# Optimization experiments

Measured on AMD Instinct MI355X. Metric: run time of the kernel, lower is better.

Reference implementation:

```python
import jax, jax.numpy as jnp
import numpy as np

B, NP, FIN = 128, 64, 2048   # graphs, nodes per graph, input feat
H, D = 8, 64                 # GAT heads, per-head dim
HD = H * D                   # 512
HID = 1024                   # Set2Set channels (concat of two 512 convs)
R2 = 16.0                    # radius^2 (r=4)
SLOPE = 0.2                  # GATConv leaky_relu slope
EPS = 0.1                    # BatchNorm eps


def setup_inputs() -> dict:
    key = jax.random.key(0)
    ks = jax.random.split(key, 20)
    s = 0.02
    inp = {}
    inp['x'] = jax.random.normal(ks[0], (B * NP, FIN), jnp.float32)
    inp['pos'] = jax.random.uniform(ks[1], (B * NP, 2), jnp.float32) * 20.0
    inp['batch'] = jnp.repeat(jnp.arange(B, dtype=jnp.int32), NP)
    # lin01: Linear(2048,2048,bias=False) + BN(2048, eps=0.1) (eval mode)
    inp['W0'] = jax.random.normal(ks[2], (FIN, 2048), jnp.float32) * s
    inp['bn0_g'] = jnp.ones((2048,), jnp.float32)
    inp['bn0_b'] = jnp.zeros((2048,), jnp.float32)
    inp['bn0_m'] = jnp.zeros((2048,), jnp.float32)
    inp['bn0_v'] = jnp.ones((2048,), jnp.float32)
    # two GATConv(2048, 64, heads=8)
    inp['Wg1'] = jax.random.normal(ks[3], (2048, HD), jnp.float32) * s
    inp['as1'] = jax.random.normal(ks[4], (H, D), jnp.float32) * s
    inp['ad1'] = jax.random.normal(ks[5], (H, D), jnp.float32) * s
    inp['b1'] = jnp.zeros((HD,), jnp.float32)
    inp['Wg2'] = jax.random.normal(ks[6], (2048, HD), jnp.float32) * s
    inp['as2'] = jax.random.normal(ks[7], (H, D), jnp.float32) * s
    inp['ad2'] = jax.random.normal(ks[8], (H, D), jnp.float32) * s
    inp['b2'] = jnp.zeros((HD,), jnp.float32)
    # Set2Set LSTM: 2 layers, input 2*HID, hidden HID
    inp['Wih0'] = jax.random.normal(ks[9], (4 * HID, 2 * HID), jnp.float32) * s
    inp['Whh0'] = jax.random.normal(ks[10], (4 * HID, HID), jnp.float32) * s
    inp['bih0'] = jnp.zeros((4 * HID,), jnp.float32)
    inp['bhh0'] = jnp.zeros((4 * HID,), jnp.float32)
    inp['Wih1'] = jax.random.normal(ks[11], (4 * HID, HID), jnp.float32) * s
    inp['Whh1'] = jax.random.normal(ks[12], (4 * HID, HID), jnp.float32) * s
    inp['bih1'] = jnp.zeros((4 * HID,), jnp.float32)
    inp['bhh1'] = jnp.zeros((4 * HID,), jnp.float32)
    # lin2: Linear(2048,1024,bias=False) + BN(1024, eps=0.1)
    inp['W2'] = jax.random.normal(ks[13], (2 * HID, HID), jnp.float32) * s
    inp['bn2_g'] = jnp.ones((HID,), jnp.float32)
    inp['bn2_b'] = jnp.zeros((HID,), jnp.float32)
    inp['bn2_m'] = jnp.zeros((HID,), jnp.float32)
    inp['bn2_v'] = jnp.ones((HID,), jnp.float32)
    # lin3: Linear(1024, 10)
    inp['W3'] = jax.random.normal(ks[14], (HID, 10), jnp.float32) * s
    inp['b3'] = jnp.zeros((10,), jnp.float32)
    return inp


def _bn(x, g, b, m, v):
    return (x - m) * jax.lax.rsqrt(v + EPS) * g + b


def _gat(xb, adj, Wg, a_src, a_dst, bias):
    # xb: [B, NP, 2048], adj: [B, NP, NP] bool (diag True = self-loops)
    h = (xb @ Wg).reshape(B, NP, H, D)
    es = jnp.einsum('bnhd,hd->bnh', h, a_src)   # source-node score
    ed = jnp.einsum('bnhd,hd->bnh', h, a_dst)   # target-node score
    # e[b, i, j, h]: edge j -> i
    e = jax.nn.leaky_relu(ed[:, :, None, :] + es[:, None, :, :], SLOPE)
    e = jnp.where(adj[..., None], e, -jnp.inf)
    alpha = jax.nn.softmax(e, axis=2)           # softmax over neighbors j
    out = jnp.einsum('bijh,bjhd->bihd', alpha, h).reshape(B, NP, HD)
    return out + bias


def _cell(inp, h, c, Wih, Whh, bih, bhh):
    z = inp @ Wih.T + h @ Whh.T + bih + bhh
    i, f, g, o = jnp.split(z, 4, axis=-1)
    c = jax.nn.sigmoid(f) * c + jax.nn.sigmoid(i) * jnp.tanh(g)
    return jax.nn.sigmoid(o) * jnp.tanh(c), c


def _forward(x, pos, W0, bn0_g, bn0_b, bn0_m, bn0_v,
             Wg1, as1, ad1, b1, Wg2, as2, ad2, b2,
             Wih0, Whh0, bih0, bhh0, Wih1, Whh1, bih1, bhh1,
             W2, bn2_g, bn2_b, bn2_m, bn2_v, W3, b3):
    # radius_graph(r=4) per graph; GATConv re-adds self-loops -> diag True
    p = pos.reshape(B, NP, 2)
    d2 = jnp.sum((p[:, :, None, :] - p[:, None, :, :]) ** 2, axis=-1)
    adj = d2 <= R2
    x = _bn(jax.nn.relu(x @ W0), bn0_g, bn0_b, bn0_m, bn0_v)  # dropout: eval
    xb = x.reshape(B, NP, 2048)
    g1 = jax.nn.relu(_gat(xb, adj, Wg1, as1, ad1, b1))
    g2 = jax.nn.relu(_gat(xb, adj, Wg2, as2, ad2, b2))
    x2 = jnp.concatenate([g1, g2], axis=-1)                   # [B, NP, 1024]
    # Set2Set: processing_steps=2, 2-layer LSTM
    q_star = jnp.zeros((B, 2 * HID), x2.dtype)
    h0 = c0 = h1 = c1 = jnp.zeros((B, HID), x2.dtype)
    for _ in range(2):
        h0, c0 = _cell(q_star, h0, c0, Wih0, Whh0, bih0, bhh0)
        h1, c1 = _cell(h0, h1, c1, Wih1, Whh1, bih1, bhh1)
        e = jnp.einsum('bnd,bd->bn', x2, h1)
        a = jax.nn.softmax(e, axis=1)                         # per-graph softmax
        r = jnp.einsum('bn,bnd->bd', a, x2)
        q_star = jnp.concatenate([h1, r], axis=-1)            # [B, 2048]
    y = _bn(jax.nn.relu(q_star @ W2), bn2_g, bn2_b, bn2_m, bn2_v)
    return y @ W3 + b3                                        # [B, 10] ('A2')


def reference(x, pos, batch, W0, bn0_g, bn0_b, bn0_m, bn0_v,
              Wg1, as1, ad1, b1, Wg2, as2, ad2, b2,
              Wih0, Whh0, bih0, bhh0, Wih1, Whh1, bih1, bhh1,
              W2, bn2_g, bn2_b, bn2_m, bn2_v, W3, b3):
    # batch ids are implicit in the fixed [B, NP] layout
    return _forward(x, pos, W0, bn0_g, bn0_b, bn0_m, bn0_v,
                    Wg1, as1, ad1, b1, Wg2, as2, ad2, b2,
                    Wih0, Whh0, bih0, bhh0, Wih1, Whh1, bih1, bhh1,
                    W2, bn2_g, bn2_b, bn2_m, bn2_v, W3, b3)
```

## Files before the change

kernel.cpp:

```cpp
#include <hip/hip_runtime.h>
#include <hip/hip_bf16.h>

typedef unsigned short u16;
typedef __attribute__((ext_vector_type(8))) short short8;
typedef __attribute__((ext_vector_type(4))) float f32x4;
typedef unsigned long long u64;

#define DI __device__ __forceinline__

DI u16 f2b(float f){
  unsigned u = __float_as_uint(f);
  unsigned r = 0x7fffu + ((u >> 16) & 1u);
  return (u16)((u + r) >> 16);
}
DI float b2f(u16 u){ return __uint_as_float((unsigned)u << 16); }

DI void gl_lds16(const void* g, void* l){
  __builtin_amdgcn_global_load_lds((const __attribute__((address_space(1))) void*)g,
                                   (__attribute__((address_space(3))) void*)l, 16, 0, 0);
}

constexpr size_t O_XBF = 0;
constexpr size_t O_W0T = O_XBF + 33554432;
constexpr size_t O_WGT = O_W0T + 8388608;
constexpr size_t O_W2T = O_WGT + 4194304;
constexpr size_t O_LW0 = O_W2T + 4194304;
constexpr size_t O_LW1 = O_LW0 + 25165824;
constexpr size_t O_XB  = O_LW1 + 16777216;
constexpr size_t O_H   = O_XB  + 33554432;
constexpr size_t O_ES  = O_H   + 33554432;
constexpr size_t O_ED  = O_ES  + 524288;
constexpr size_t O_ADJ = O_ED  + 524288;
constexpr size_t O_SC0 = O_ADJ + 65536;
constexpr size_t O_SH0 = O_SC0 + 8192;
constexpr size_t O_SC2 = O_SH0 + 8192;
constexpr size_t O_SH2 = O_SC2 + 4096;
constexpr size_t O_LB0 = O_SH2 + 4096;
constexpr size_t O_LB1 = O_LB0 + 16384;
constexpr size_t S_AC0 = 0;
constexpr size_t S_AC1 = S_AC0 + 786432;
constexpr size_t S_C0  = S_AC1 + 524288;
constexpr size_t S_C1  = S_C0  + 524288;
constexpr size_t S_H1F = S_C1  + 524288;
constexpr size_t S_ZP  = S_H1F + 524288;
constexpr size_t S_E   = S_ZP  + 16777216;
constexpr size_t S_H0U = S_E   + 32768;
constexpr size_t S_Z1U = S_H0U + 4096;

__global__ __launch_bounds__(256) void cvt_big(
    const float* __restrict__ x, const float* __restrict__ Wih0, const float* __restrict__ Whh0,
    const float* __restrict__ Wih1, const float* __restrict__ Whh1,
    u16* __restrict__ xbf, u16* __restrict__ lw0, u16* __restrict__ lw1){
  int bx = blockIdx.x;
  int idx, cq, dld, doff;
  const float* src; u16* dst;
  if(bx < 16384){      src = x;    dst = xbf; idx = bx * 256 + threadIdx.x;            cq = 512; dld = 2048; doff = 0; }
  else if(bx < 24576){ src = Wih0; dst = lw0; idx = (bx - 16384) * 256 + threadIdx.x;  cq = 512; dld = 3072; doff = 0; }
  else if(bx < 28672){ src = Whh0; dst = lw0; idx = (bx - 24576) * 256 + threadIdx.x;  cq = 256; dld = 3072; doff = 2048; }
  else if(bx < 32768){ src = Wih1; dst = lw1; idx = (bx - 28672) * 256 + threadIdx.x;  cq = 256; dld = 2048; doff = 0; }
  else {               src = Whh1; dst = lw1; idx = (bx - 32768) * 256 + threadIdx.x;  cq = 256; dld = 2048; doff = 1024; }
  int r = idx / cq, c4 = (idx - r * cq) << 2;
  float4 v = *(const float4*)(src + (size_t)r * (cq << 2) + c4);
  u16 o[4] = { f2b(v.x), f2b(v.y), f2b(v.z), f2b(v.w) };
  *(ushort4*)(dst + (size_t)r * dld + doff + c4) = *(ushort4*)o;
}

__global__ void cvt_tr(const float* __restrict__ W0, const float* __restrict__ Wg1,
                       const float* __restrict__ Wg2, const float* __restrict__ W2,
                       u16* __restrict__ w0t, u16* __restrict__ wgt, u16* __restrict__ w2t){
  __shared__ float tile[32][33];
  int bx = blockIdx.x;
  const float* src; u16* dst; int C, droff;
  if(bx < 64){      src = W0;  dst = w0t; C = 2048; droff = 0; }
  else if(bx < 80){ src = Wg1; dst = wgt; C = 512;  droff = 0;   bx -= 64; }
  else if(bx < 96){ src = Wg2; dst = wgt; C = 512;  droff = 512; bx -= 80; }
  else {            src = W2;  dst = w2t; C = 1024; droff = 0;   bx -= 96; }
  int c0 = bx * 32, r0 = blockIdx.y * 32;
  int tx = threadIdx.x, ty = threadIdx.y;
  for(int i = 0; i < 4; i++)
    tile[ty + 8*i][tx] = src[(size_t)(r0 + ty + 8*i) * C + c0 + tx];
  __syncthreads();
  for(int i = 0; i < 4; i++)
    dst[(size_t)(droff + c0 + ty + 8*i) * 2048 + r0 + tx] = f2b(tile[tx][ty + 8*i]);
}

__global__ void prep(const float* g0, const float* b0, const float* m0, const float* v0,
                     const float* g2, const float* b2, const float* m2, const float* v2,
                     const float* bih0, const float* bhh0, const float* bih1, const float* bhh1,
                     float* sc0, float* sh0, float* sc2, float* sh2, float* lb0, float* lb1){
  int t = blockIdx.x * 256 + threadIdx.x;
  if(t < 2048){ float s = g0[t] * rsqrtf(v0[t] + 0.1f); sc0[t] = s; sh0[t] = b0[t] - m0[t] * s; }
  if(t < 1024){ float s = g2[t] * rsqrtf(v2[t] + 0.1f); sc2[t] = s; sh2[t] = b2[t] - m2[t] * s; }
  if(t < 4096){ lb0[t] = bih0[t] + bhh0[t]; lb1[t] = bih1[t] + bhh1[t]; }
}

__global__ void adj_kernel(const float* __restrict__ pos, u64* __restrict__ adjm){
  int b = blockIdx.x, l = threadIdx.x;
  __shared__ float px[64], py[64];
  float2 p = ((const float2*)pos)[b * 64 + l];
  px[l] = p.x; py[l] = p.y;
  __syncthreads();
  float xi = px[l], yi = py[l];
  u64 m = 0;
  for(int j = 0; j < 64; j++){
    float dx = xi - px[j], dy = yi - py[j];
    if(dx * dx + dy * dy <= 16.0f) m |= (1ull << j);
  }
  adjm[b * 64 + l] = m;
}

template<int MODE>
__global__ __launch_bounds__(256) void gemm_bf16(
    const u16* __restrict__ A, const u16* __restrict__ Bt,
    float* __restrict__ Cf, u16* __restrict__ Cb,
    const float* __restrict__ p1, const float* __restrict__ p2,
    int M, int N, int K)
{
  constexpr int BM = 128, BN = 128, BK = 64;
  __shared__ alignas(16) u16 Al[BM * BK];
  __shared__ alignas(16) u16 Bl[BN * BK];
  int m0 = blockIdx.x * BM, n0 = blockIdx.y * BN;
  int t = threadIdx.x, w = t >> 6, l = t & 63;
  int wm = (w >> 1) * 64, wn = (w & 1) * 64;
  f32x4 acc[4][4];
  for(int a = 0; a < 4; a++) for(int b = 0; b < 4; b++) acc[a][b] = {0.f, 0.f, 0.f, 0.f};

  const short8* Ap = (const short8*)Al;
  const short8* Bp = (const short8*)Bl;

  for(int k0 = 0; k0 < K; k0 += BK){
    #pragma unroll
    for(int u = t; u < BM * 8; u += 256){
      int r = u >> 3, c = u & 7;
      gl_lds16(A + (size_t)(m0 + r) * K + k0 + ((c ^ (r & 7)) << 3), Al + u * 8);
    }
    #pragma unroll
    for(int u = t; u < BN * 8; u += 256){
      int r = u >> 3, c = u & 7;
      gl_lds16(Bt + (size_t)(n0 + r) * K + k0 + ((c ^ (r & 7)) << 3), Bl + u * 8);
    }
    __syncthreads();
    #pragma unroll
    for(int ks = 0; ks < 2; ks++){
      int kc = ks * 4 + (l >> 4);
      short8 av[4], bv[4];
      #pragma unroll
      for(int mi = 0; mi < 4; mi++){ int r = wm + mi * 16 + (l & 15); av[mi] = Ap[r * 8 + (kc ^ (r & 7))]; }
      #pragma unroll
      for(int ni = 0; ni < 4; ni++){ int r = wn + ni * 16 + (l & 15); bv[ni] = Bp[r * 8 + (kc ^ (r & 7))]; }
      #pragma unroll
      for(int mi = 0; mi < 4; mi++)
        #pragma unroll
        for(int ni = 0; ni < 4; ni++)
          acc[mi][ni] = __builtin_amdgcn_mfma_f32_16x16x32_bf16(av[mi], bv[ni], acc[mi][ni], 0, 0, 0);
    }
    __syncthreads();
  }

  int cr = m0 + wm + ((l >> 4) << 2);
  int cc = n0 + wn + (l & 15);
  for(int mi = 0; mi < 4; mi++)
    for(int ni = 0; ni < 4; ni++)
      for(int r = 0; r < 4; r++){
        int row = cr + mi * 16 + r, col = cc + ni * 16;
        float v = acc[mi][ni][r];
        if(MODE == 1){ v = fmaxf(v, 0.f) * p1[col] + p2[col]; Cb[(size_t)row * N + col] = f2b(v); }
        else if(MODE == 3){ Cb[(size_t)row * N + col] = f2b(v); }
        else { Cf[(size_t)row * N + col] = v; }
      }
}

__global__ __launch_bounds__(256) void gemm_sk(
    const u16* __restrict__ A, const u16* __restrict__ Bt, float* __restrict__ Cf,
    int N, int lda, int ldb, int kPer)
{
  constexpr int BM = 128, BN = 64, BK = 64;
  __shared__ alignas(16) u16 Al[BM * BK];
  __shared__ alignas(16) u16 Bl[BN * BK];
  int n0 = blockIdx.x * BN;
  int kb = blockIdx.y * kPer;
  float* C = Cf + (size_t)blockIdx.y * 128 * N;
  int t = threadIdx.x, w = t >> 6, l = t & 63;
  int wm = (w >> 1) * 64, wn = (w & 1) * 32;
  f32x4 acc[4][2];
  for(int a = 0; a < 4; a++) for(int b = 0; b < 2; b++) acc[a][b] = {0.f, 0.f, 0.f, 0.f};

  const short8* Ap = (const short8*)Al;
  const short8* Bp = (const short8*)Bl;

  for(int k0 = kb; k0 < kb + kPer; k0 += BK){
    #pragma unroll
    for(int u = t; u < BM * 8; u += 256){
      int r = u >> 3, c = u & 7;
      gl_lds16(A + (size_t)r * lda + k0 + ((c ^ (r & 7)) << 3), Al + u * 8);
    }
    #pragma unroll
    for(int u = t; u < BN * 8; u += 256){
      int r = u >> 3, c = u & 7;
      gl_lds16(Bt + (size_t)(n0 + r) * ldb + k0 + ((c ^ (r & 7)) << 3), Bl + u * 8);
    }
    __syncthreads();
    #pragma unroll
    for(int ks = 0; ks < 2; ks++){
      int kc = ks * 4 + (l >> 4);
      short8 av[4], bv[2];
      #pragma unroll
      for(int mi = 0; mi < 4; mi++){ int r = wm + mi * 16 + (l & 15); av[mi] = Ap[r * 8 + (kc ^ (r & 7))]; }
      #pragma unroll
      for(int ni = 0; ni < 2; ni++){ int r = wn + ni * 16 + (l & 15); bv[ni] = Bp[r * 8 + (kc ^ (r & 7))]; }
      #pragma unroll
      for(int mi = 0; mi < 4; mi++)
        #pragma unroll
        for(int ni = 0; ni < 2; ni++)
          acc[mi][ni] = __builtin_amdgcn_mfma_f32_16x16x32_bf16(av[mi], bv[ni], acc[mi][ni], 0, 0, 0);
    }
    __syncthreads();
  }

  int cr = wm + ((l >> 4) << 2);
  int cc = n0 + wn + (l & 15);
  for(int mi = 0; mi < 4; mi++)
    for(int ni = 0; ni < 2; ni++)
      for(int r = 0; r < 4; r++)
        C[(size_t)(cr + mi * 16 + r) * N + cc + ni * 16] = acc[mi][ni][r];
}

__global__ __launch_bounds__(256) void gat_scores(const u16* __restrict__ h,
    const float* __restrict__ as1, const float* __restrict__ ad1,
    const float* __restrict__ as2, const float* __restrict__ ad2,
    float* __restrict__ es, float* __restrict__ ed){
  __shared__ float aS[16][64], aD[16][64];
  int t = threadIdx.x;
  for(int i = t; i < 1024; i += 256){
    int cc = i >> 6, d = i & 63;
    aS[cc][d] = (cc < 8) ? as1[i] : as2[i - 512];
    aD[cc][d] = (cc < 8) ? ad1[i] : ad2[i - 512];
  }
  __syncthreads();
  int w = t >> 6, l = t & 63;
  int node = blockIdx.x * 4 + w;
  const u16* hr = h + (size_t)node * 1024;
  for(int cc = 0; cc < 16; cc++){
    float v = b2f(hr[cc * 64 + l]);
    float ps = v * aS[cc][l], pd = v * aD[cc][l];
    for(int o = 32; o; o >>= 1){ ps += __shfl_down(ps, o); pd += __shfl_down(pd, o); }
    if(l == 0){ es[node * 16 + cc] = ps; ed[node * 16 + cc] = pd; }
  }
}

__global__ __launch_bounds__(256) void gat_attn2(const u64* __restrict__ adjm,
    const float* __restrict__ es, const float* __restrict__ ed,
    const u16* __restrict__ h, const float* __restrict__ b1, const float* __restrict__ b2,
    float* __restrict__ x2){
  int b = blockIdx.x;
  int cv = blockIdx.y >> 3, hh = blockIdx.y & 7;
  __shared__ float hst[64][64];
  __shared__ float alphaL[64][65];
  __shared__ float esl[64], edl[64];
  __shared__ u64 adjs[64];
  int t = threadIdx.x, w = t >> 6, l = t & 63;
  {
    int j = t >> 2, d0 = (t & 3) * 16;
    const u16* hr = h + (size_t)(b * 64 + j) * 1024 + cv * 512 + hh * 64 + d0;
    #pragma unroll
    for(int k = 0; k < 16; k++) hst[j][d0 + k] = b2f(hr[k]);
  }
  if(t < 64){
    esl[t] = es[(b * 64 + t) * 16 + cv * 8 + hh];
    edl[t] = ed[(b * 64 + t) * 16 + cv * 8 + hh];
    adjs[t] = adjm[b * 64 + t];
  }
  __syncthreads();
  for(int it = 0; it < 16; it++){
    int i = it * 4 + w;
    bool on = (adjs[i] >> l) & 1;
    float e = edl[i] + esl[l];
    e = e > 0.f ? e : 0.2f * e;
    float mx = on ? e : -1e30f;
    for(int o = 32; o; o >>= 1) mx = fmaxf(mx, __shfl_xor(mx, o));
    float p = on ? __expf(e - mx) : 0.f;
    float s = p;
    for(int o = 32; o; o >>= 1) s += __shfl_xor(s, o);
    alphaL[i][l] = p / s;
  }
  __syncthreads();
  int i = t >> 2, q = t & 3;
  float acc[16];
  #pragma unroll
  for(int k = 0; k < 16; k++) acc[k] = 0.f;
  for(int j = 0; j < 64; j++){
    float al = alphaL[i][j];
    const float* hr = &hst[j][q * 16];
    #pragma unroll
    for(int k = 0; k < 16; k++) acc[k] += al * hr[k];
  }
  const float* bias = (cv ? b2 : b1) + hh * 64 + q * 16;
  float* op = x2 + (size_t)(b * 64 + i) * 1024 + cv * 512 + hh * 64 + q * 16;
  #pragma unroll
  for(int k = 0; k < 16; k += 4){
    float4 o;
    o.x = fmaxf(acc[k] + bias[k], 0.f);
    o.y = fmaxf(acc[k+1] + bias[k+1], 0.f);
    o.z = fmaxf(acc[k+2] + bias[k+2], 0.f);
    o.w = fmaxf(acc[k+3] + bias[k+3], 0.f);
    *(float4*)(op + k) = o;
  }
}

__global__ void s2s0_h0(const float* __restrict__ lb0, float* __restrict__ h0u){
  int j = blockIdx.x * 256 + threadIdx.x;
  if(j >= 1024) return;
  float zi = lb0[j], zg = lb0[2048 + j], zo = lb0[3072 + j];
  float si = 1.f / (1.f + __expf(-zi));
  float so = 1.f / (1.f + __expf(-zo));
  float cn = si * tanhf(zg);
  h0u[j] = so * tanhf(cn);
}

__global__ __launch_bounds__(256) void s2s0_gemv(const float* __restrict__ Wih1,
    const float* __restrict__ lb1, const float* __restrict__ h0u, float* __restrict__ z1u){
  __shared__ float hs[1024];
  int t = threadIdx.x;
  for(int i = t; i < 1024; i += 256) hs[i] = h0u[i];
  __syncthreads();
  int w = t >> 6, l = t & 63;
  int r = blockIdx.x * 4 + w;
  const float* wr = Wih1 + (size_t)r * 1024;
  float s = 0.f;
  #pragma unroll
  for(int k = 0; k < 16; k++) s += wr[l + 64 * k] * hs[l + 64 * k];
  for(int o = 32; o; o >>= 1) s += __shfl_xor(s, o);
  if(l == 0) z1u[r] = s + lb1[r];
}

__global__ void s2s0_bcast(const float* __restrict__ lb0, const float* __restrict__ z1u,
    float* __restrict__ c0b, float* __restrict__ c1b, float* __restrict__ h1f,
    u16* __restrict__ ac0, u16* __restrict__ ac1){
  int t = blockIdx.x * 256 + threadIdx.x;
  int b = t >> 10, j = t & 1023;
  float zi0 = lb0[j], zg0 = lb0[2048 + j], zo0 = lb0[3072 + j];
  float c0 = (1.f / (1.f + __expf(-zi0))) * tanhf(zg0);
  float h0 = (1.f / (1.f + __expf(-zo0))) * tanhf(c0);
  float zi1 = z1u[j], zg1 = z1u[2048 + j], zo1 = z1u[3072 + j];
  float c1 = (1.f / (1.f + __expf(-zi1))) * tanhf(zg1);
  float h1 = (1.f / (1.f + __expf(-zo1))) * tanhf(c1);
  c0b[t] = c0;
  c1b[t] = c1;
  h1f[t] = h1;
  u16 h0b = f2b(h0), h1b = f2b(h1);
  ac0[(size_t)b * 3072 + j] = h1b;
  ac0[(size_t)b * 3072 + 2048 + j] = h0b;
  ac1[(size_t)b * 2048 + j] = h0b;
  ac1[(size_t)b * 2048 + 1024 + j] = h1b;
}

__global__ void lstm_gate0(const float* __restrict__ zp, const float* __restrict__ lb,
                           float* __restrict__ c, u16* __restrict__ ac0, u16* __restrict__ ac1,
                           int ns){
  int t = blockIdx.x * 256 + threadIdx.x;
  int b = t >> 10, j = t & 1023;
  size_t base = (size_t)b * 4096;
  float zi = 0, zf = 0, zg = 0, zo = 0;
  for(int s = 0; s < ns; s++){
    const float* zr = zp + (size_t)s * 524288 + base;
    zi += zr[j]; zf += zr[1024 + j]; zg += zr[2048 + j]; zo += zr[3072 + j];
  }
  zi += lb[j]; zf += lb[1024 + j]; zg += lb[2048 + j]; zo += lb[3072 + j];
  float ci = c[t];
  float si = 1.f / (1.f + __expf(-zi)), sf = 1.f / (1.f + __expf(-zf)), so = 1.f / (1.f + __expf(-zo));
  float cn = sf * ci + si * tanhf(zg);
  c[t] = cn;
  u16 hb = f2b(so * tanhf(cn));
  ac0[(size_t)b * 3072 + 2048 + j] = hb;
  ac1[(size_t)b * 2048 + j] = hb;
}

__global__ void lstm_gate1(const float* __restrict__ zp, const float* __restrict__ lb,
                           float* __restrict__ c, float* __restrict__ h1f,
                           u16* __restrict__ ac1, u16* __restrict__ ac0, int ns){
  int t = blockIdx.x * 256 + threadIdx.x;
  int b = t >> 10, j = t & 1023;
  size_t base = (size_t)b * 4096;
  float zi = 0, zf = 0, zg = 0, zo = 0;
  for(int s = 0; s < ns; s++){
    const float* zr = zp + (size_t)s * 524288 + base;
    zi += zr[j]; zf += zr[1024 + j]; zg += zr[2048 + j]; zo += zr[3072 + j];
  }
  zi += lb[j]; zf += lb[1024 + j]; zg += lb[2048 + j]; zo += lb[3072 + j];
  float ci = c[t];
  float si = 1.f / (1.f + __expf(-zi)), sf = 1.f / (1.f + __expf(-zf)), so = 1.f / (1.f + __expf(-zo));
  float cn = sf * ci + si * tanhf(zg);
  c[t] = cn;
  float hn = so * tanhf(cn);
  h1f[t] = hn;
  u16 hb = f2b(hn);
  ac1[(size_t)b * 2048 + 1024 + j] = hb;
  ac0[(size_t)b * 3072 + j] = hb;
}

__global__ __launch_bounds__(256) void s2s_e(const float* __restrict__ x2,
    const float* __restrict__ h1, float* __restrict__ e){
  int t = threadIdx.x, w = t >> 6, l = t & 63;
  int node = blockIdx.x * 4 + w;
  int b = node >> 6;
  const float4* xr = (const float4*)(x2 + (size_t)node * 1024);
  const float4* hr = (const float4*)(h1 + (size_t)b * 1024);
  float s = 0.f;
  #pragma unroll
  for(int k = 0; k < 4; k++){
    float4 a = xr[l + 64 * k], c = hr[l + 64 * k];
    s += a.x * c.x + a.y * c.y + a.z * c.z + a.w * c.w;
  }
  for(int o = 32; o; o >>= 1) s += __shfl_xor(s, o);
  if(l == 0) e[node] = s;
}

__global__ __launch_bounds__(256) void s2s_r(const float* __restrict__ x2,
    const float* __restrict__ e, u16* __restrict__ ac0){
  int b = blockIdx.x, sl = blockIdx.y;
  __shared__ float al[64];
  int t = threadIdx.x;
  if(t < 64){
    float v = e[b * 64 + t];
    float mx = v;
    for(int o = 32; o; o >>= 1) mx = fmaxf(mx, __shfl_xor(mx, o));
    float p = __expf(v - mx);
    float ss = p;
    for(int o = 32; o; o >>= 1) ss += __shfl_xor(ss, o);
    al[t] = p / ss;
  }
  __syncthreads();
  int d = sl * 256 + t;
  const float* xp = x2 + (size_t)b * 64 * 1024 + d;
  float r = 0.f;
  #pragma unroll 8
  for(int j = 0; j < 64; j++) r += al[j] * xp[j * 1024];
  ac0[(size_t)b * 3072 + 1024 + d] = f2b(r);
}

__global__ __launch_bounds__(256) void lin3(const float* __restrict__ zp2,
    const float* __restrict__ sc2, const float* __restrict__ sh2,
    const float* __restrict__ W3, const float* __restrict__ b3, float* __restrict__ out){
  int b = blockIdx.x;
  __shared__ float yl[1024];
  int t = threadIdx.x, w = t >> 6, l = t & 63;
  for(int d = t; d < 1024; d += 256){
    float v = 0.f;
    for(int s = 0; s < 8; s++) v += zp2[(size_t)s * 131072 + b * 1024 + d];
    yl[d] = fmaxf(v, 0.f) * sc2[d] + sh2[d];
  }
  __syncthreads();
  for(int n = w; n < 10; n += 4){
    float s = 0.f;
    for(int d = l; d < 1024; d += 64) s += yl[d] * W3[d * 10 + n];
    for(int o = 32; o; o >>= 1) s += __shfl_xor(s, o);
    if(l == 0) out[b * 10 + n] = s + b3[n];
  }
}

extern "C" void kernel_launch(void* const* d_in, const int* in_sizes, int n_in,
                              void* d_out, int out_size, void* d_ws, size_t ws_size,
                              hipStream_t stream){
  const float* x    = (const float*)d_in[0];
  const float* pos  = (const float*)d_in[1];
  const float* W0   = (const float*)d_in[3];
  const float* bn0g = (const float*)d_in[4];
  const float* bn0b = (const float*)d_in[5];
  const float* bn0m = (const float*)d_in[6];
  const float* bn0v = (const float*)d_in[7];
  const float* Wg1  = (const float*)d_in[8];
  const float* as1  = (const float*)d_in[9];
  const float* ad1  = (const float*)d_in[10];
  const float* b1   = (const float*)d_in[11];
  const float* Wg2  = (const float*)d_in[12];
  const float* as2  = (const float*)d_in[13];
  const float* ad2  = (const float*)d_in[14];
  const float* b2   = (const float*)d_in[15];
  const float* Wih0 = (const float*)d_in[16];
  const float* Whh0 = (const float*)d_in[17];
  const float* bih0 = (const float*)d_in[18];
  const float* bhh0 = (const float*)d_in[19];
  const float* Wih1 = (const float*)d_in[20];
  const float* Whh1 = (const float*)d_in[21];
  const float* bih1 = (const float*)d_in[22];
  const float* bhh1 = (const float*)d_in[23];
  const float* W2   = (const float*)d_in[24];
  const float* bn2g = (const float*)d_in[25];
  const float* bn2b = (const float*)d_in[26];
  const float* bn2m = (const float*)d_in[27];
  const float* bn2v = (const float*)d_in[28];
  const float* W3   = (const float*)d_in[29];
  const float* b3   = (const float*)d_in[30];

  char* ws = (char*)d_ws;
  u16*   xbf  = (u16*)(ws + O_XBF);
  float* x2   = (float*)(ws + O_XBF);
  u16*   w0t  = (u16*)(ws + O_W0T);
  u16*   wgt  = (u16*)(ws + O_WGT);
  u16*   w2t  = (u16*)(ws + O_W2T);
  u16*   lw0  = (u16*)(ws + O_LW0);
  u16*   lw1  = (u16*)(ws + O_LW1);
  u16*   xb   = (u16*)(ws + O_XB);
  u16*   hb   = (u16*)(ws + O_H);
  float* es   = (float*)(ws + O_ES);
  float* ed   = (float*)(ws + O_ED);
  u64*   adjm = (u64*)(ws + O_ADJ);
  float* sc0  = (float*)(ws + O_SC0);
  float* sh0  = (float*)(ws + O_SH0);
  float* sc2  = (float*)(ws + O_SC2);
  float* sh2  = (float*)(ws + O_SH2);
  float* lb0  = (float*)(ws + O_LB0);
  float* lb1  = (float*)(ws + O_LB1);
  char*  s2sb = ws + O_H;
  u16*   ac0  = (u16*)(s2sb + S_AC0);
  u16*   ac1  = (u16*)(s2sb + S_AC1);
  float* c0b  = (float*)(s2sb + S_C0);
  float* c1b  = (float*)(s2sb + S_C1);
  float* h1f  = (float*)(s2sb + S_H1F);
  float* zp   = (float*)(s2sb + S_ZP);
  float* ebuf = (float*)(s2sb + S_E);
  float* h0u  = (float*)(s2sb + S_H0U);
  float* z1u  = (float*)(s2sb + S_Z1U);

  prep<<<16, 256, 0, stream>>>(bn0g, bn0b, bn0m, bn0v, bn2g, bn2b, bn2m, bn2v,
                               bih0, bhh0, bih1, bhh1, sc0, sh0, sc2, sh2, lb0, lb1);
  adj_kernel<<<128, 64, 0, stream>>>(pos, adjm);
  cvt_big<<<36864, 256, 0, stream>>>(x, Wih0, Whh0, Wih1, Whh1, xbf, lw0, lw1);
  cvt_tr<<<dim3(128, 64), dim3(32, 8), 0, stream>>>(W0, Wg1, Wg2, W2, w0t, wgt, w2t);

  gemm_bf16<1><<<dim3(64, 16), 256, 0, stream>>>(xbf, w0t, nullptr, xb, sc0, sh0, 8192, 2048, 2048);
  gemm_bf16<3><<<dim3(64, 8), 256, 0, stream>>>(xb, wgt, nullptr, hb, nullptr, nullptr, 8192, 1024, 2048);
  gat_scores<<<2048, 256, 0, stream>>>(hb, as1, ad1, as2, ad2, es, ed);
  gat_attn2<<<dim3(128, 16), 256, 0, stream>>>(adjm, es, ed, hb, b1, b2, x2);

  s2s0_h0<<<4, 256, 0, stream>>>(lb0, h0u);
  s2s0_gemv<<<1024, 256, 0, stream>>>(Wih1, lb1, h0u, z1u);
  s2s0_bcast<<<512, 256, 0, stream>>>(lb0, z1u, c0b, c1b, h1f, ac0, ac1);
  s2s_e<<<2048, 256, 0, stream>>>(x2, h1f, ebuf);
  s2s_r<<<dim3(128, 4), 256, 0, stream>>>(x2, ebuf, ac0);

  gemm_sk<<<dim3(64, 8), 256, 0, stream>>>(ac0, lw0, zp, 4096, 3072, 3072, 384);
  lstm_gate0<<<512, 256, 0, stream>>>(zp, lb0, c0b, ac0, ac1, 8);
  gemm_sk<<<dim3(64, 8), 256, 0, stream>>>(ac1, lw1, zp, 4096, 2048, 2048, 256);
  lstm_gate1<<<512, 256, 0, stream>>>(zp, lb1, c1b, h1f, ac1, ac0, 8);
  s2s_e<<<2048, 256, 0, stream>>>(x2, h1f, ebuf);
  s2s_r<<<dim3(128, 4), 256, 0, stream>>>(x2, ebuf, ac0);

  gemm_sk<<<dim3(16, 8), 256, 0, stream>>>(ac0, w2t, zp, 1024, 3072, 2048, 256);
  lin3<<<128, 256, 0, stream>>>(zp, sc2, sh2, W3, b3, (float*)d_out);
}
```

Baseline: 340.4 us.

## Fuse LSTM weight bf16 conversion into split-K GEMM and store GAT output as bf16

Drops the separate pass that converted the LSTM weight matrices to bf16. A new split-K GEMM loads the fp32 Wih/Whh weights directly, converts them in registers and writes them into LDS. This removes a large convert-and-write step and the re-read of its output. The GAT attention output x2 is now stored as bf16, which halves the traffic for the Set2Set e/r kernels but adds rounding error. The new B load is synchronous and uses two float4 loads per 16 bytes of bf16, which may slow the GEMM's inner loop.

```diff
diff --git a/kernel.cpp b/kernel.cpp
--- a/kernel.cpp
+++ b/kernel.cpp
@@ -24,9 +24,7 @@
 constexpr size_t O_W0T = O_XBF + 33554432;
 constexpr size_t O_WGT = O_W0T + 8388608;
 constexpr size_t O_W2T = O_WGT + 4194304;
-constexpr size_t O_LW0 = O_W2T + 4194304;
-constexpr size_t O_LW1 = O_LW0 + 25165824;
-constexpr size_t O_XB  = O_LW1 + 16777216;
+constexpr size_t O_XB  = O_W2T + 4194304;
 constexpr size_t O_H   = O_XB  + 33554432;
 constexpr size_t O_ES  = O_H   + 33554432;
 constexpr size_t O_ED  = O_ES  + 524288;
@@ -47,22 +45,12 @@
 constexpr size_t S_H0U = S_E   + 32768;
 constexpr size_t S_Z1U = S_H0U + 4096;
 
-__global__ __launch_bounds__(256) void cvt_big(
-    const float* __restrict__ x, const float* __restrict__ Wih0, const float* __restrict__ Whh0,
-    const float* __restrict__ Wih1, const float* __restrict__ Whh1,
-    u16* __restrict__ xbf, u16* __restrict__ lw0, u16* __restrict__ lw1){
-  int bx = blockIdx.x;
-  int idx, cq, dld, doff;
-  const float* src; u16* dst;
-  if(bx < 16384){      src = x;    dst = xbf; idx = bx * 256 + threadIdx.x;            cq = 512; dld = 2048; doff = 0; }
-  else if(bx < 24576){ src = Wih0; dst = lw0; idx = (bx - 16384) * 256 + threadIdx.x;  cq = 512; dld = 3072; doff = 0; }
-  else if(bx < 28672){ src = Whh0; dst = lw0; idx = (bx - 24576) * 256 + threadIdx.x;  cq = 256; dld = 3072; doff = 2048; }
-  else if(bx < 32768){ src = Wih1; dst = lw1; idx = (bx - 28672) * 256 + threadIdx.x;  cq = 256; dld = 2048; doff = 0; }
-  else {               src = Whh1; dst = lw1; idx = (bx - 32768) * 256 + threadIdx.x;  cq = 256; dld = 2048; doff = 1024; }
-  int r = idx / cq, c4 = (idx - r * cq) << 2;
-  float4 v = *(const float4*)(src + (size_t)r * (cq << 2) + c4);
+__global__ __launch_bounds__(256) void cvt_x(const float* __restrict__ x, u16* __restrict__ xbf){
+  int idx = blockIdx.x * 256 + threadIdx.x;
+  int r = idx >> 9, c4 = (idx & 511) << 2;
+  float4 v = *(const float4*)(x + (size_t)r * 2048 + c4);
   u16 o[4] = { f2b(v.x), f2b(v.y), f2b(v.z), f2b(v.w) };
-  *(ushort4*)(dst + (size_t)r * dld + doff + c4) = *(ushort4*)o;
+  *(ushort4*)(xbf + (size_t)r * 2048 + c4) = *(ushort4*)o;
 }
 
 __global__ void cvt_tr(const float* __restrict__ W0, const float* __restrict__ Wg1,
@@ -225,6 +213,69 @@
         C[(size_t)(cr + mi * 16 + r) * N + cc + ni * 16] = acc[mi][ni][r];
 }
 
+__global__ __launch_bounds__(256) void gemm_skf(
+    const u16* __restrict__ A, const float* __restrict__ Wih, const float* __restrict__ Whh,
+    float* __restrict__ Cf, int N, int lda, int Kih, int Khh, int kPer)
+{
+  constexpr int BM = 128, BN = 64, BK = 64;
+  __shared__ alignas(16) u16 Al[BM * BK];
+  __shared__ alignas(16) u16 Bl[BN * BK];
+  int n0 = blockIdx.x * BN;
+  int kb = blockIdx.y * kPer;
+  float* C = Cf + (size_t)blockIdx.y * 128 * N;
+  int t = threadIdx.x, w = t >> 6, l = t & 63;
+  int wm = (w >> 1) * 64, wn = (w & 1) * 32;
+  f32x4 acc[4][2];
+  for(int a = 0; a < 4; a++) for(int b = 0; b < 2; b++) acc[a][b] = {0.f, 0.f, 0.f, 0.f};
+
+  const short8* Ap = (const short8*)Al;
+  const short8* Bp = (const short8*)Bl;
+
+  for(int k0 = kb; k0 < kb + kPer; k0 += BK){
+    #pragma unroll
+    for(int u = t; u < BM * 8; u += 256){
+      int r = u >> 3, c = u & 7;
+      gl_lds16(A + (size_t)r * lda + k0 + ((c ^ (r & 7)) << 3), Al + u * 8);
+    }
+    #pragma unroll
+    for(int u = t; u < BN * 8; u += 256){
+      int r = u >> 3, c = u & 7;
+      int gk = k0 + c * 8;
+      const float* src = (gk < Kih) ? (Wih + (size_t)(n0 + r) * Kih + gk)
+                                    : (Whh + (size_t)(n0 + r) * Khh + (gk - Kih));
+      float4 v0 = *(const float4*)src;
+      float4 v1 = *(const float4*)(src + 4);
+      short8 ov;
+      ov[0] = (short)f2b(v0.x); ov[1] = (short)f2b(v0.y); ov[2] = (short)f2b(v0.z); ov[3] = (short)f2b(v0.w);
+      ov[4] = (short)f2b(v1.x); ov[5] = (short)f2b(v1.y); ov[6] = (short)f2b(v1.z); ov[7] = (short)f2b(v1.w);
+      ((short8*)Bl)[r * 8 + (c ^ (r & 7))] = ov;
+    }
+    __syncthreads();
+    #pragma unroll
+    for(int ks = 0; ks < 2; ks++){
+      int kc = ks * 4 + (l >> 4);
+      short8 av[4], bv[2];
+      #pragma unroll
+      for(int mi = 0; mi < 4; mi++){ int r = wm + mi * 16 + (l & 15); av[mi] = Ap[r * 8 + (kc ^ (r & 7))]; }
+      #pragma unroll
+      for(int ni = 0; ni < 2; ni++){ int r = wn + ni * 16 + (l & 15); bv[ni] = Bp[r * 8 + (kc ^ (r & 7))]; }
+      #pragma unroll
+      for(int mi = 0; mi < 4; mi++)
+        #pragma unroll
+        for(int ni = 0; ni < 2; ni++)
+          acc[mi][ni] = __builtin_amdgcn_mfma_f32_16x16x32_bf16(av[mi], bv[ni], acc[mi][ni], 0, 0, 0);
+    }
+    __syncthreads();
+  }
+
+  int cr = wm + ((l >> 4) << 2);
+  int cc = n0 + wn + (l & 15);
+  for(int mi = 0; mi < 4; mi++)
+    for(int ni = 0; ni < 2; ni++)
+      for(int r = 0; r < 4; r++)
+        C[(size_t)(cr + mi * 16 + r) * N + cc + ni * 16] = acc[mi][ni][r];
+}
+
 __global__ __launch_bounds__(256) void gat_scores(const u16* __restrict__ h,
     const float* __restrict__ as1, const float* __restrict__ ad1,
     const float* __restrict__ as2, const float* __restrict__ ad2,
@@ -251,7 +302,7 @@
 __global__ __launch_bounds__(256) void gat_attn2(const u64* __restrict__ adjm,
     const float* __restrict__ es, const float* __restrict__ ed,
     const u16* __restrict__ h, const float* __restrict__ b1, const float* __restrict__ b2,
-    float* __restrict__ x2){
+    u16* __restrict__ x2b){
   int b = blockIdx.x;
   int cv = blockIdx.y >> 3, hh = blockIdx.y & 7;
   __shared__ float hst[64][64];
@@ -295,16 +346,9 @@
     for(int k = 0; k < 16; k++) acc[k] += al * hr[k];
   }
   const float* bias = (cv ? b2 : b1) + hh * 64 + q * 16;
-  float* op = x2 + (size_t)(b * 64 + i) * 1024 + cv * 512 + hh * 64 + q * 16;
+  u16* op = x2b + (size_t)(b * 64 + i) * 1024 + cv * 512 + hh * 64 + q * 16;
   #pragma unroll
-  for(int k = 0; k < 16; k += 4){
-    float4 o;
-    o.x = fmaxf(acc[k] + bias[k], 0.f);
-    o.y = fmaxf(acc[k+1] + bias[k+1], 0.f);
-    o.z = fmaxf(acc[k+2] + bias[k+2], 0.f);
-    o.w = fmaxf(acc[k+3] + bias[k+3], 0.f);
-    *(float4*)(op + k) = o;
-  }
+  for(int k = 0; k < 16; k++) op[k] = f2b(fmaxf(acc[k] + bias[k], 0.f));
 }
 
 __global__ void s2s0_h0(const float* __restrict__ lb0, float* __restrict__ h0u){
@@ -398,24 +442,24 @@
   ac0[(size_t)b * 3072 + j] = hb;
 }
 
-__global__ __launch_bounds__(256) void s2s_e(const float* __restrict__ x2,
+__global__ __launch_bounds__(256) void s2s_e(const u16* __restrict__ x2b,
     const float* __restrict__ h1, float* __restrict__ e){
   int t = threadIdx.x, w = t >> 6, l = t & 63;
   int node = blockIdx.x * 4 + w;
   int b = node >> 6;
-  const float4* xr = (const float4*)(x2 + (size_t)node * 1024);
-  const float4* hr = (const float4*)(h1 + (size_t)b * 1024);
+  const u16* xr = x2b + (size_t)node * 1024;
+  const float* hr = h1 + (size_t)b * 1024;
   float s = 0.f;
   #pragma unroll
-  for(int k = 0; k < 4; k++){
-    float4 a = xr[l + 64 * k], c = hr[l + 64 * k];
-    s += a.x * c.x + a.y * c.y + a.z * c.z + a.w * c.w;
+  for(int k = 0; k < 16; k++){
+    int d = k * 64 + l;
+    s += b2f(xr[d]) * hr[d];
   }
   for(int o = 32; o; o >>= 1) s += __shfl_xor(s, o);
   if(l == 0) e[node] = s;
 }
 
-__global__ __launch_bounds__(256) void s2s_r(const float* __restrict__ x2,
+__global__ __launch_bounds__(256) void s2s_r(const u16* __restrict__ x2b,
     const float* __restrict__ e, u16* __restrict__ ac0){
   int b = blockIdx.x, sl = blockIdx.y;
   __shared__ float al[64];
@@ -431,10 +475,10 @@
   }
   __syncthreads();
   int d = sl * 256 + t;
-  const float* xp = x2 + (size_t)b * 64 * 1024 + d;
+  const u16* xp = x2b + (size_t)b * 65536 + d;
   float r = 0.f;
   #pragma unroll 8
-  for(int j = 0; j < 64; j++) r += al[j] * xp[j * 1024];
+  for(int j = 0; j < 64; j++) r += al[j] * b2f(xp[j * 1024]);
   ac0[(size_t)b * 3072 + 1024 + d] = f2b(r);
 }
 
@@ -494,12 +538,10 @@
 
   char* ws = (char*)d_ws;
   u16*   xbf  = (u16*)(ws + O_XBF);
-  float* x2   = (float*)(ws + O_XBF);
+  u16*   x2b  = (u16*)(ws + O_XBF);
   u16*   w0t  = (u16*)(ws + O_W0T);
   u16*   wgt  = (u16*)(ws + O_WGT);
   u16*   w2t  = (u16*)(ws + O_W2T);
-  u16*   lw0  = (u16*)(ws + O_LW0);
-  u16*   lw1  = (u16*)(ws + O_LW1);
   u16*   xb   = (u16*)(ws + O_XB);
   u16*   hb   = (u16*)(ws + O_H);
   float* es   = (float*)(ws + O_ES);
@@ -525,26 +567,26 @@
   prep<<<16, 256, 0, stream>>>(bn0g, bn0b, bn0m, bn0v, bn2g, bn2b, bn2m, bn2v,
                                bih0, bhh0, bih1, bhh1, sc0, sh0, sc2, sh2, lb0, lb1);
   adj_kernel<<<128, 64, 0, stream>>>(pos, adjm);
-  cvt_big<<<36864, 256, 0, stream>>>(x, Wih0, Whh0, Wih1, Whh1, xbf, lw0, lw1);
+  cvt_x<<<16384, 256, 0, stream>>>(x, xbf);
   cvt_tr<<<dim3(128, 64), dim3(32, 8), 0, stream>>>(W0, Wg1, Wg2, W2, w0t, wgt, w2t);
 
   gemm_bf16<1><<<dim3(64, 16), 256, 0, stream>>>(xbf, w0t, nullptr, xb, sc0, sh0, 8192, 2048, 2048);
   gemm_bf16<3><<<dim3(64, 8), 256, 0, stream>>>(xb, wgt, nullptr, hb, nullptr, nullptr, 8192, 1024, 2048);
   gat_scores<<<2048, 256, 0, stream>>>(hb, as1, ad1, as2, ad2, es, ed);
-  gat_attn2<<<dim3(128, 16), 256, 0, stream>>>(adjm, es, ed, hb, b1, b2, x2);
+  gat_attn2<<<dim3(128, 16), 256, 0, stream>>>(adjm, es, ed, hb, b1, b2, x2b);
 
   s2s0_h0<<<4, 256, 0, stream>>>(lb0, h0u);
   s2s0_gemv<<<1024, 256, 0, stream>>>(Wih1, lb1, h0u, z1u);
   s2s0_bcast<<<512, 256, 0, stream>>>(lb0, z1u, c0b, c1b, h1f, ac0, ac1);
-  s2s_e<<<2048, 256, 0, stream>>>(x2, h1f, ebuf);
-  s2s_r<<<dim3(128, 4), 256, 0, stream>>>(x2, ebuf, ac0);
-
-  gemm_sk<<<dim3(64, 8), 256, 0, stream>>>(ac0, lw0, zp, 4096, 3072, 3072, 384);
+  s2s_e<<<2048, 256, 0, stream>>>(x2b, h1f, ebuf);
+  s2s_r<<<dim3(128, 4), 256, 0, stream>>>(x2b, ebuf, ac0);
+
+  gemm_skf<<<dim3(64, 8), 256, 0, stream>>>(ac0, Wih0, Whh0, zp, 4096, 3072, 2048, 1024, 384);
   lstm_gate0<<<512, 256, 0, stream>>>(zp, lb0, c0b, ac0, ac1, 8);
-  gemm_sk<<<dim3(64, 8), 256, 0, stream>>>(ac1, lw1, zp, 4096, 2048, 2048, 256);
+  gemm_skf<<<dim3(64, 8), 256, 0, stream>>>(ac1, Wih1, Whh1, zp, 4096, 2048, 1024, 1024, 256);
   lstm_gate1<<<512, 256, 0, stream>>>(zp, lb1, c1b, h1f, ac1, ac0, 8);
-  s2s_e<<<2048, 256, 0, stream>>>(x2, h1f, ebuf);
-  s2s_r<<<dim3(128, 4), 256, 0, stream>>>(x2, ebuf, ac0);
+  s2s_e<<<2048, 256, 0, stream>>>(x2b, h1f, ebuf);
+  s2s_r<<<dim3(128, 4), 256, 0, stream>>>(x2b, ebuf, ac0);
 
   gemm_sk<<<dim3(16, 8), 256, 0, stream>>>(ac0, w2t, zp, 1024, 3072, 2048, 256);
   lin3<<<128, 256, 0, stream>>>(zp, sc2, sh2, W3, b3, (float*)d_out);
```

Measured after the change: 318.6 us. 1.07x faster.
